# Performance work log

Hardware: AMD Instinct MI355X
Metric: run time of the kernel (lower is better)

## Reference

```python
import jax, jax.numpy as jnp
import numpy as np

B, C, H, W = 4, 256, 64, 64
G, K, P = 4, 7, 3          # groups, kernel size, padding
RED = 32                   # out_channels // reduce_ratio
BN_EPS = 1e-5


def setup_inputs() -> dict:
    key = jax.random.key(0)
    ks = jax.random.split(key, 3)
    x = jax.random.normal(ks[0], (B, C, H, W), dtype=jnp.float32)
    w_reduce = jax.random.normal(ks[1], (RED, C), dtype=jnp.float32) * (1.0 / np.sqrt(C))
    bn_gamma = jnp.ones((RED,), dtype=jnp.float32)
    bn_beta = jnp.zeros((RED,), dtype=jnp.float32)
    w_span = jax.random.normal(ks[2], (K * K * G, RED), dtype=jnp.float32) * (1.0 / np.sqrt(RED))
    b_span = jnp.zeros((K * K * G,), dtype=jnp.float32)
    return {"x": x, "w_reduce": w_reduce, "bn_gamma": bn_gamma,
            "bn_beta": bn_beta, "w_span": w_span, "b_span": b_span}


def _involution(x, w_reduce, bn_gamma, bn_beta, w_span, b_span):
    # ---- dynamic kernel generation (stride=1 so AvgPool is identity) ----
    red = jnp.einsum('oc,bchw->bohw', w_reduce, x)                 # [B,RED,H,W]
    # BatchNorm2d forward with batch statistics (training-mode math)
    mean = red.mean(axis=(0, 2, 3), keepdims=True)
    var = red.var(axis=(0, 2, 3), keepdims=True)
    red_n = (red - mean) * jax.lax.rsqrt(var + BN_EPS)
    act = jax.nn.relu(red_n * bn_gamma[None, :, None, None] + bn_beta[None, :, None, None])
    ker = jnp.einsum('oc,bchw->bohw', w_span, act) + b_span[None, :, None, None]
    ker = ker.reshape(B, G, K * K, H, W)                           # [B,G,KK,H,W]

    # ---- unfold: K*K shifted views of the padded input ----
    xp = jnp.pad(x, ((0, 0), (0, 0), (P, P), (P, P)))
    patches = jnp.stack([xp[:, :, i:i + H, j:j + W]
                         for i in range(K) for j in range(K)], axis=2)  # [B,C,KK,H,W]
    patches = patches.reshape(B, G, C // G, K * K, H, W)

    # ---- per-pixel weighted neighborhood sum ----
    out = jnp.einsum('bgkhw,bgckhw->bgchw', ker, patches)
    return out.reshape(B, C, H, W)


def reference(x, w_reduce, bn_gamma, bn_beta, w_span, b_span):
    return _involution(x, w_reduce, bn_gamma, bn_beta, w_span, b_span)
```

## Files before the change

kernel.cpp:

```cpp
#include <hip/hip_runtime.h>

#define B_ 4
#define C_ 256
#define H_ 64
#define W_ 64
#define HW_ 4096
#define G_ 4
#define K_ 7
#define P_ 3
#define KK_ 49
#define KKG_ 196
#define RED_ 32
#define NPIX_ 16384
#define NSTAT_ 16384.0f
#define BN_EPS_ 1e-5f
#define OCH_ 28

#define CPB_ 8
#define TH_ 8
#define TRS_ 14
#define TRW_ 76

__global__ __launch_bounds__(256) void k_reduce(const float* __restrict__ x,
                                               const float* __restrict__ wr,
                                               float4* __restrict__ part,
                                               float* __restrict__ gstats) {
    __shared__ float wlds[8 * 64];
    const int tid = threadIdx.x;
    const int og  = blockIdx.y;
    const int bz  = blockIdx.z;
    if (blockIdx.x == 0 && og == 0 && bz == 0 && tid < 64) gstats[tid] = 0.0f;
    for (int i = tid; i < 512; i += 256) {
        const int oi = i >> 6, cc = i & 63;
        wlds[i] = wr[(og * 8 + oi) * C_ + bz * 64 + cc];
    }
    __syncthreads();

    const int p2 = blockIdx.x * 256 + tid;
    const int b  = p2 >> 11;
    const int hw = (p2 & 2047) << 1;
    const float* xp = x + ((size_t)(b * C_ + bz * 64)) * HW_ + hw;

    float a[8][2];
#pragma unroll
    for (int oi = 0; oi < 8; ++oi) { a[oi][0] = 0.f; a[oi][1] = 0.f; }

#pragma unroll 8
    for (int cc = 0; cc < 64; ++cc) {
        const float2 v = *(const float2*)(xp + (size_t)cc * HW_);
#pragma unroll
        for (int oi = 0; oi < 8; ++oi) {
            const float wv = wlds[oi * 64 + cc];
            a[oi][0] = fmaf(wv, v.x, a[oi][0]);
            a[oi][1] = fmaf(wv, v.y, a[oi][1]);
        }
    }

    const int slot = bz * 4 + og;
    float4* pp0 = part + (((size_t)(slot * 2 + 0)) << 14) + (p2 << 1);
    float4* pp1 = part + (((size_t)(slot * 2 + 1)) << 14) + (p2 << 1);
    pp0[0] = make_float4(a[0][0], a[1][0], a[2][0], a[3][0]);
    pp0[1] = make_float4(a[0][1], a[1][1], a[2][1], a[3][1]);
    pp1[0] = make_float4(a[4][0], a[5][0], a[6][0], a[7][0]);
    pp1[1] = make_float4(a[4][1], a[5][1], a[6][1], a[7][1]);
}

__global__ __launch_bounds__(256) void k_comb(const float4* __restrict__ part,
                                              float4* __restrict__ red,
                                              float* __restrict__ gsum,
                                              float* __restrict__ gsq) {
    __shared__ float lsum[4][8];
    const int tid  = threadIdx.x;
    const int lane = tid & 63;
    const int wv   = tid >> 6;
    const int oq   = blockIdx.y;
    const int og   = oq >> 1;
    const int half = oq & 1;
    const int p    = blockIdx.x * 256 + tid;

    float4 s = make_float4(0.f, 0.f, 0.f, 0.f);
#pragma unroll
    for (int bz = 0; bz < 4; ++bz) {
        const float4 v = part[(((size_t)((bz * 4 + og) * 2 + half)) << 14) + p];
        s.x += v.x; s.y += v.y; s.z += v.z; s.w += v.w;
    }
    red[((size_t)oq << 14) + p] = s;

    float s0 = s.x, s1 = s.y, s2 = s.z, s3 = s.w;
    float q0 = s.x*s.x, q1 = s.y*s.y, q2 = s.z*s.z, q3 = s.w*s.w;
#pragma unroll
    for (int off = 32; off > 0; off >>= 1) {
        s0 += __shfl_down(s0, off);  q0 += __shfl_down(q0, off);
        s1 += __shfl_down(s1, off);  q1 += __shfl_down(q1, off);
        s2 += __shfl_down(s2, off);  q2 += __shfl_down(q2, off);
        s3 += __shfl_down(s3, off);  q3 += __shfl_down(q3, off);
    }
    if (lane == 0) {
        lsum[wv][0] = s0; lsum[wv][1] = s1; lsum[wv][2] = s2; lsum[wv][3] = s3;
        lsum[wv][4] = q0; lsum[wv][5] = q1; lsum[wv][6] = q2; lsum[wv][7] = q3;
    }
    __syncthreads();
    if (tid < 8) {
        const float v = lsum[0][tid] + lsum[1][tid] + lsum[2][tid] + lsum[3][tid];
        float* dst = (tid < 4) ? &gsum[oq * 4 + tid] : &gsq[oq * 4 + (tid - 4)];
        atomicAdd(dst, v);
    }
}

__global__ __launch_bounds__(256) void k_span(const float4* __restrict__ red,
                                              const float* __restrict__ wspan,
                                              const float* __restrict__ bspan,
                                              const float* __restrict__ gsum,
                                              const float* __restrict__ gsq,
                                              const float* __restrict__ gamma,
                                              const float* __restrict__ beta,
                                              float* __restrict__ ker) {
    __shared__ float wlds[OCH_ * RED_];
    __shared__ float sc_l[RED_], sh_l[RED_], bs_l[OCH_];
    const int tid   = threadIdx.x;
    const int chunk = blockIdx.y;
    const int obase = chunk * OCH_;
    for (int i = tid; i < OCH_ * RED_; i += 256) wlds[i] = wspan[obase * RED_ + i];
    if (tid < RED_) {
        const float m   = gsum[tid] * (1.0f / NSTAT_);
        const float var = gsq[tid] * (1.0f / NSTAT_) - m * m;
        const float inv = rsqrtf(var + BN_EPS_);
        const float sc  = gamma[tid] * inv;
        sc_l[tid] = sc;
        sh_l[tid] = beta[tid] - m * sc;
    }
    if (tid < OCH_) bs_l[tid] = bspan[obase + tid];
    __syncthreads();

    const int p  = blockIdx.x * 256 + tid;
    const int b  = p >> 12;
    const int hw = p & 4095;

    float act[RED_];
#pragma unroll
    for (int og = 0; og < 8; ++og) {
        const float4 v = red[((size_t)og << 14) + p];
        act[4*og+0] = v.x; act[4*og+1] = v.y; act[4*og+2] = v.z; act[4*og+3] = v.w;
    }
#pragma unroll
    for (int o = 0; o < RED_; ++o)
        act[o] = fmaxf(fmaf(act[o], sc_l[o], sh_l[o]), 0.0f);

    float* kp = ker + ((size_t)b * KKG_ + obase) * HW_ + hw;
#pragma unroll 4
    for (int o = 0; o < OCH_; ++o) {
        float s = bs_l[o];
#pragma unroll
        for (int c = 0; c < RED_; ++c)
            s = fmaf(wlds[o * RED_ + c], act[c], s);
        kp[(size_t)o * HW_] = s;
    }
}

__global__ __launch_bounds__(256) void k_inv(const float* __restrict__ x,
                                             const float* __restrict__ ker,
                                             float* __restrict__ out) {
    __shared__ float tile[CPB_][TRS_][TRW_];
    const int tid = threadIdx.x;
    const int wg  = tid & 7;
    const int hq  = (tid >> 3) & 7;
    const int cq  = tid >> 6;
    const int bx  = blockIdx.x;
    const int ht  = bx & 7;
    const int cblk = (bx >> 3) & 31;
    const int b   = bx >> 8;
    const int h0  = ht << 3;
    const int c0  = cblk << 3;
    const int g   = c0 >> 6;
    const int w0  = wg << 3;
    const int h   = h0 + hq;

    const float4 fz = make_float4(0.f, 0.f, 0.f, 0.f);
#pragma unroll
    for (int it = 0; it < 7; ++it) {
        const int i   = it * 256 + tid;
        const int ci  = i / (TRS_ * 16);
        const int rem = i - ci * (TRS_ * 16);
        const int r   = rem >> 4;
        const int seg = rem & 15;
        const int hh  = h0 + r - P_;
        float4 v = fz;
        if (hh >= 0 && hh < H_)
            v = *(const float4*)(x + (((size_t)(b * C_ + c0 + ci)) << 12) + (hh << 6) + (seg << 2));
        *(float4*)&tile[ci][r][4 + (seg << 2)] = v;
    }
    if (tid < CPB_ * TRS_ * 2) {
        const int ci  = tid / (TRS_ * 2);
        const int rem = tid - ci * (TRS_ * 2);
        const int r   = rem >> 1;
        *(float4*)&tile[ci][r][(rem & 1) ? 68 : 0] = fz;
    }
    __syncthreads();

    const int cA = cq << 1;
    const float* kp = ker + (((size_t)b * KKG_ + g * KK_) << 12) + (h << 6) + w0;

    float accA[8], accB[8];
#pragma unroll
    for (int dw = 0; dw < 8; ++dw) { accA[dw] = 0.f; accB[dw] = 0.f; }

#pragma unroll
    for (int i = 0; i < K_; ++i) {
        const int r = hq + i;
        float wa[16], wb[16];
        const float* ta = &tile[cA][r][w0];
        const float* tb = &tile[cA + 1][r][w0];
#pragma unroll
        for (int t = 0; t < 4; ++t) {
            const float4 va = *(const float4*)(ta + (t << 2));
            const float4 vb = *(const float4*)(tb + (t << 2));
            wa[4*t+0]=va.x; wa[4*t+1]=va.y; wa[4*t+2]=va.z; wa[4*t+3]=va.w;
            wb[4*t+0]=vb.x; wb[4*t+1]=vb.y; wb[4*t+2]=vb.z; wb[4*t+3]=vb.w;
        }
#pragma unroll
        for (int j = 0; j < K_; ++j) {
            const float* kpp = kp + ((size_t)(i * K_ + j) << 12);
            const float4 k0 = *(const float4*)kpp;
            const float4 k1 = *(const float4*)(kpp + 4);
            const float kv[8] = {k0.x, k0.y, k0.z, k0.w, k1.x, k1.y, k1.z, k1.w};
#pragma unroll
            for (int dw = 0; dw < 8; ++dw) {
                accA[dw] = fmaf(kv[dw], wa[dw + j + 1], accA[dw]);
                accB[dw] = fmaf(kv[dw], wb[dw + j + 1], accB[dw]);
            }
        }
    }

    float* oA = out + (((size_t)(b * C_ + c0 + cA)) << 12) + (h << 6) + w0;
    *(float4*)(oA)     = make_float4(accA[0], accA[1], accA[2], accA[3]);
    *(float4*)(oA + 4) = make_float4(accA[4], accA[5], accA[6], accA[7]);
    float* oB = oA + HW_;
    *(float4*)(oB)     = make_float4(accB[0], accB[1], accB[2], accB[3]);
    *(float4*)(oB + 4) = make_float4(accB[4], accB[5], accB[6], accB[7]);
}

extern "C" void kernel_launch(void* const* d_in, const int* in_sizes, int n_in,
                              void* d_out, int out_size, void* d_ws, size_t ws_size,
                              hipStream_t stream) {
    const float* x     = (const float*)d_in[0];
    const float* wr    = (const float*)d_in[1];
    const float* gamma = (const float*)d_in[2];
    const float* beta  = (const float*)d_in[3];
    const float* wspan = (const float*)d_in[4];
    const float* bspan = (const float*)d_in[5];
    float* out = (float*)d_out;
    float* ws  = (float*)d_ws;

    float* red   = ws;
    float* gsum  = ws + 524288;
    float* gsq   = gsum + 32;
    float* ker   = ws + 524416;
    float* part  = ker;

    hipLaunchKernelGGL(k_reduce, dim3(32, 4, 4),  dim3(256), 0, stream, x, wr, (float4*)part, gsum);
    hipLaunchKernelGGL(k_comb,   dim3(64, 8),     dim3(256), 0, stream, (const float4*)part, (float4*)red, gsum, gsq);
    hipLaunchKernelGGL(k_span,   dim3(64, 7),     dim3(256), 0, stream, (const float4*)red, wspan, bspan, gsum, gsq, gamma, beta, ker);
    hipLaunchKernelGGL(k_inv,    dim3(1024),      dim3(256), 0, stream, x, ker, out);
}
```

Measured before the change: 63.34 us.

## Retile reduce and involution kernels: more outputs per thread, shorter row tiles

```diff
diff --git a/kernel.cpp b/kernel.cpp
--- a/kernel.cpp
+++ b/kernel.cpp
@@ -16,53 +16,48 @@
 #define BN_EPS_ 1e-5f
 #define OCH_ 28
 
-#define CPB_ 8
-#define TH_ 8
-#define TRS_ 14
+#define CPB_ 16
+#define TH_ 4
+#define TRS_ 10
 #define TRW_ 76
 
 __global__ __launch_bounds__(256) void k_reduce(const float* __restrict__ x,
                                                const float* __restrict__ wr,
                                                float4* __restrict__ part,
                                                float* __restrict__ gstats) {
-    __shared__ float wlds[8 * 64];
+    __shared__ float wlds[16 * 64];
     const int tid = threadIdx.x;
     const int og  = blockIdx.y;
     const int bz  = blockIdx.z;
     if (blockIdx.x == 0 && og == 0 && bz == 0 && tid < 64) gstats[tid] = 0.0f;
-    for (int i = tid; i < 512; i += 256) {
+    for (int i = tid; i < 1024; i += 256) {
         const int oi = i >> 6, cc = i & 63;
-        wlds[i] = wr[(og * 8 + oi) * C_ + bz * 64 + cc];
-    }
-    __syncthreads();
-
-    const int p2 = blockIdx.x * 256 + tid;
-    const int b  = p2 >> 11;
-    const int hw = (p2 & 2047) << 1;
+        wlds[i] = wr[(og * 16 + oi) * C_ + bz * 64 + cc];
+    }
+    __syncthreads();
+
+    const int p  = blockIdx.x * 256 + tid;
+    const int b  = p >> 12;
+    const int hw = p & 4095;
     const float* xp = x + ((size_t)(b * C_ + bz * 64)) * HW_ + hw;
 
-    float a[8][2];
-#pragma unroll
-    for (int oi = 0; oi < 8; ++oi) { a[oi][0] = 0.f; a[oi][1] = 0.f; }
+    float a[16];
+#pragma unroll
+    for (int oi = 0; oi < 16; ++oi) a[oi] = 0.0f;
 
 #pragma unroll 8
     for (int cc = 0; cc < 64; ++cc) {
-        const float2 v = *(const float2*)(xp + (size_t)cc * HW_);
-#pragma unroll
-        for (int oi = 0; oi < 8; ++oi) {
-            const float wv = wlds[oi * 64 + cc];
-            a[oi][0] = fmaf(wv, v.x, a[oi][0]);
-            a[oi][1] = fmaf(wv, v.y, a[oi][1]);
-        }
-    }
-
-    const int slot = bz * 4 + og;
-    float4* pp0 = part + (((size_t)(slot * 2 + 0)) << 14) + (p2 << 1);
-    float4* pp1 = part + (((size_t)(slot * 2 + 1)) << 14) + (p2 << 1);
-    pp0[0] = make_float4(a[0][0], a[1][0], a[2][0], a[3][0]);
-    pp0[1] = make_float4(a[0][1], a[1][1], a[2][1], a[3][1]);
-    pp1[0] = make_float4(a[4][0], a[5][0], a[6][0], a[7][0]);
-    pp1[1] = make_float4(a[4][1], a[5][1], a[6][1], a[7][1]);
+        const float v = xp[(size_t)cc * HW_];
+#pragma unroll
+        for (int oi = 0; oi < 16; ++oi)
+            a[oi] = fmaf(wlds[oi * 64 + cc], v, a[oi]);
+    }
+
+    const int sbase = (bz * 2 + og) * 4;
+#pragma unroll
+    for (int q = 0; q < 4; ++q)
+        part[(((size_t)(sbase + q)) << 14) + p] =
+            make_float4(a[4*q], a[4*q+1], a[4*q+2], a[4*q+3]);
 }
 
 __global__ __launch_bounds__(256) void k_comb(const float4* __restrict__ part,
@@ -74,14 +69,14 @@
     const int lane = tid & 63;
     const int wv   = tid >> 6;
     const int oq   = blockIdx.y;
-    const int og   = oq >> 1;
-    const int half = oq & 1;
+    const int og   = oq >> 2;
+    const int q    = oq & 3;
     const int p    = blockIdx.x * 256 + tid;
 
     float4 s = make_float4(0.f, 0.f, 0.f, 0.f);
 #pragma unroll
     for (int bz = 0; bz < 4; ++bz) {
-        const float4 v = part[(((size_t)((bz * 4 + og) * 2 + half)) << 14) + p];
+        const float4 v = part[(((size_t)((bz * 2 + og) * 4 + q)) << 14) + p];
         s.x += v.x; s.y += v.y; s.z += v.z; s.w += v.w;
     }
     red[((size_t)oq << 14) + p] = s;
@@ -163,21 +158,21 @@
     __shared__ float tile[CPB_][TRS_][TRW_];
     const int tid = threadIdx.x;
     const int wg  = tid & 7;
-    const int hq  = (tid >> 3) & 7;
-    const int cq  = tid >> 6;
+    const int hq  = (tid >> 3) & 3;
+    const int cq  = tid >> 5;
     const int bx  = blockIdx.x;
-    const int ht  = bx & 7;
-    const int cblk = (bx >> 3) & 31;
+    const int ht  = bx & 15;
+    const int cblk = (bx >> 4) & 15;
     const int b   = bx >> 8;
-    const int h0  = ht << 3;
-    const int c0  = cblk << 3;
+    const int h0  = ht << 2;
+    const int c0  = cblk << 4;
     const int g   = c0 >> 6;
     const int w0  = wg << 3;
     const int h   = h0 + hq;
 
     const float4 fz = make_float4(0.f, 0.f, 0.f, 0.f);
 #pragma unroll
-    for (int it = 0; it < 7; ++it) {
+    for (int it = 0; it < 10; ++it) {
         const int i   = it * 256 + tid;
         const int ci  = i / (TRS_ * 16);
         const int rem = i - ci * (TRS_ * 16);
@@ -189,9 +184,9 @@
             v = *(const float4*)(x + (((size_t)(b * C_ + c0 + ci)) << 12) + (hh << 6) + (seg << 2));
         *(float4*)&tile[ci][r][4 + (seg << 2)] = v;
     }
-    if (tid < CPB_ * TRS_ * 2) {
-        const int ci  = tid / (TRS_ * 2);
-        const int rem = tid - ci * (TRS_ * 2);
+    for (int i = tid; i < CPB_ * TRS_ * 2; i += 256) {
+        const int ci  = i / (TRS_ * 2);
+        const int rem = i - ci * (TRS_ * 2);
         const int r   = rem >> 1;
         *(float4*)&tile[ci][r][(rem & 1) ? 68 : 0] = fz;
     }
@@ -257,7 +252,7 @@
     float* ker   = ws + 524416;
     float* part  = ker;
 
-    hipLaunchKernelGGL(k_reduce, dim3(32, 4, 4),  dim3(256), 0, stream, x, wr, (float4*)part, gsum);
+    hipLaunchKernelGGL(k_reduce, dim3(64, 2, 4),  dim3(256), 0, stream, x, wr, (float4*)part, gsum);
     hipLaunchKernelGGL(k_comb,   dim3(64, 8),     dim3(256), 0, stream, (const float4*)part, (float4*)red, gsum, gsq);
     hipLaunchKernelGGL(k_span,   dim3(64, 7),     dim3(256), 0, stream, (const float4*)red, wspan, bspan, gsum, gsq, gamma, beta, ker);
     hipLaunchKernelGGL(k_inv,    dim3(1024),      dim3(256), 0, stream, x, ker, out);
```

Result: slower. 67.60 us (+6.7%).
